# Optimization experiments

Measured on AMD Instinct MI355X. Metric: run time of the kernel, lower is better.

The kernel has to match this reference:

```python
import jax, jax.numpy as jnp
import numpy as np

N_NODES = 32768
N_EDGES = 524288
HID = 128


def _linear_params(key, fan_in, fan_out):
    kw, kb = jax.random.split(key)
    bound = 1.0 / np.sqrt(fan_in)
    w = jax.random.uniform(kw, (fan_in, fan_out), jnp.float32, -bound, bound)
    b = jax.random.uniform(kb, (fan_out,), jnp.float32, -bound, bound)
    return w, b


def setup_inputs() -> dict:
    key = jax.random.key(0)
    ks = jax.random.split(key, 8)
    x = jax.random.normal(ks[0], (N_NODES, HID), jnp.float32)
    edge_attr = jax.random.normal(ks[1], (N_EDGES, HID), jnp.float32)
    edges = jax.random.randint(ks[2], (2, N_EDGES), 0, N_NODES, jnp.int32)
    w1, b1 = _linear_params(ks[3], 3 * HID, HID)      # message_fn layer 1
    w2, b2 = _linear_params(ks[4], HID, HID)          # message_fn layer 2
    wu1, bu1 = _linear_params(ks[5], HID, 2 * HID)    # update_fn layer 1
    wu2, bu2 = _linear_params(ks[6], 2 * HID, HID)    # update_fn layer 2
    return {"x": x, "edge_attr": edge_attr, "edges": edges,
            "w1": w1, "b1": b1, "w2": w2, "b2": b2,
            "wu1": wu1, "bu1": bu1, "wu2": wu2, "bu2": bu2}


def reference(x, edge_attr, edges, w1, b1, w2, b2, wu1, bu1, wu2, bu2):
    n_nodes = x.shape[0]
    send, recv = edges[0], edges[1]
    # gather endpoint features and concat with edge attributes: [E, 3*HID]
    ea = jnp.concatenate([x[send], x[recv], edge_attr], axis=-1)
    # per-edge message MLP (Linear-SiLU-Linear-SiLU)
    h = jax.nn.silu(ea @ w1 + b1)
    msg = jax.nn.silu(h @ w2 + b2)                    # [E, HID]
    # scatter-mean into receiving nodes
    sums = jax.ops.segment_sum(msg, recv, num_segments=n_nodes)
    counts = jax.ops.segment_sum(jnp.ones((msg.shape[0],), msg.dtype), recv,
                                 num_segments=n_nodes)
    aggr = sums / jnp.maximum(counts, 1.0)[:, None]
    # residual (input_size == hidden_size -> Identity) + update MLP
    xo = x + aggr
    xo = xo + (jax.nn.silu(xo @ wu1 + bu1) @ wu2 + bu2)
    return xo, msg
```

## Files before the change

kernel.cpp:

```cpp
#include <hip/hip_runtime.h>
#include <hip/hip_bf16.h>

#define NN 32768
#define NE 524288
#define HID 128

typedef unsigned short u16;
typedef unsigned int u32;
typedef __bf16 bf16x8 __attribute__((ext_vector_type(8)));
typedef float f32x4 __attribute__((ext_vector_type(4)));

__device__ __forceinline__ u16 f2bf(float f) {
  union { float f; unsigned u; } v; v.f = f;
  return (u16)((v.u + 0x7fffu + ((v.u >> 16) & 1u)) >> 16);
}
__device__ __forceinline__ float silu_f(float v) {
  return v * __builtin_amdgcn_rcpf(1.f + __expf(-v));
}

__device__ __forceinline__ void gld16(const void* g, void* l) {
  __builtin_amdgcn_global_load_lds(
      (const __attribute__((address_space(1))) u32*)g,
      (__attribute__((address_space(3))) u32*)l, 16, 0, 0);
}

__global__ __launch_bounds__(256) void prep_k(
    const float* __restrict__ x, const float* __restrict__ w1,
    const float* __restrict__ w2, const float* __restrict__ wu1,
    const float* __restrict__ wu2,
    u16* __restrict__ xb, u16* __restrict__ w1Ts, u16* __restrict__ w2Ts,
    u16* __restrict__ wu1T, u16* __restrict__ wu2T, int* __restrict__ cnt)
{
  int i = blockIdx.x * 256 + threadIdx.x;
  xb[i] = f2bf(x[i]);
  if (i < NN) cnt[i] = 0;
  if (i < 3 * 128 * 128) {
    int j = i & 7, qs = (i >> 3) & 15, c = (i >> 7) & 127, s = i >> 14;
    int k = s * 128 + ((qs ^ (c & 7)) << 3) + j;
    w1Ts[i] = f2bf(w1[k * 128 + c]);
  }
  if (i < 128 * 128) {
    int j = i & 7, qs = (i >> 3) & 15, c = i >> 7;
    int k = ((qs ^ (c & 7)) << 3) + j;
    w2Ts[i] = f2bf(w2[k * 128 + c]);
  }
  if (i < 256 * 128) { int c = i >> 7, k = i & 127; wu1T[i] = f2bf(wu1[k * 256 + c]); }
  if (i < 128 * 256) { int c = i >> 8, k = i & 255; wu2T[i] = f2bf(wu2[k * 128 + c]); }
}

__global__ __launch_bounds__(256) void count_k(const int* __restrict__ recv,
                                               int* __restrict__ cnt)
{
  int e = blockIdx.x * 256 + threadIdx.x;
  atomicAdd(&cnt[recv[e]], 1);
}

__global__ __launch_bounds__(1024) void scan_k(const int* __restrict__ cnt,
                                               int* __restrict__ off,
                                               int* __restrict__ cursor)
{
  __shared__ int part[1024];
  const int tid = threadIdx.x;
  const int base = tid * 32;
  int v[32];
  int s = 0;
  #pragma unroll
  for (int j = 0; j < 32; ++j) { v[j] = cnt[base + j]; s += v[j]; }
  part[tid] = s;
  __syncthreads();
  #pragma unroll 1
  for (int d = 1; d < 1024; d <<= 1) {
    int t = (tid >= d) ? part[tid - d] : 0;
    __syncthreads();
    part[tid] += t;
    __syncthreads();
  }
  int ex = part[tid] - s;
  #pragma unroll
  for (int j = 0; j < 32; ++j) {
    off[base + j] = ex;
    cursor[base + j] = ex;
    ex += v[j];
  }
  if (tid == 1023) off[NN] = ex;
}

__global__ __launch_bounds__(256) void scatter_k(const int* __restrict__ recv,
                                                 int* __restrict__ cursor,
                                                 int* __restrict__ eperm)
{
  int e = blockIdx.x * 256 + threadIdx.x;
  int r = recv[e];
  int pos = atomicAdd(&cursor[r], 1);
  eperm[pos] = e;
}

__global__ __launch_bounds__(512, 4) void edge_mlp(
    const u16* __restrict__ xb, const float* __restrict__ eattr,
    const int* __restrict__ send, const int* __restrict__ recv,
    const u16* __restrict__ w1Ts, const float* __restrict__ b1,
    const u16* __restrict__ w2Ts, const float* __restrict__ b2,
    float* __restrict__ msg_out)
{
  __shared__ u16 sA[128 * 128];
  __shared__ u16 sB[128 * 128];

  const int tid  = threadIdx.x;
  const int lane = tid & 63;
  const int w    = tid >> 6;
  const int wr   = w >> 1;
  const int wc   = w & 1;
  const int fr   = lane & 15;
  const int fkq  = lane >> 4;
  const int orow = fkq * 4;
  const int e0   = blockIdx.x * 128;

  const int lrow4 = lane >> 4;
  const int schk  = lane & 15;

  int nds[4], ndr[4];
  #pragma unroll
  for (int i = 0; i < 4; ++i) {
    int e = e0 + w * 16 + i * 4 + lrow4;
    nds[i] = send[e];
    ndr[i] = recv[e];
  }

  f32x4 acc[2][4];
  #pragma unroll
  for (int m = 0; m < 2; ++m)
    #pragma unroll
    for (int n = 0; n < 4; ++n)
      #pragma unroll
      for (int r = 0; r < 4; ++r) acc[m][n][r] = 0.f;

  #pragma unroll
  for (int s = 0; s < 3; ++s) {
    if (s < 2) {
      #pragma unroll
      for (int i = 0; i < 4; ++i) {
        int rloc = w * 16 + i * 4 + lrow4;
        int node = (s == 0) ? nds[i] : ndr[i];
        gld16(xb + ((size_t)node << 7) + ((schk ^ (rloc & 7)) << 3),
              sA + ((w * 16 + i * 4) << 7));
      }
    } else {
      #pragma unroll
      for (int i = 0; i < 4; ++i) {
        int rloc = w * 16 + i * 4 + lrow4;
        int gchk = schk ^ (rloc & 7);
        const float4* p = reinterpret_cast<const float4*>(
            eattr + ((size_t)(e0 + rloc) << 7) + (gchk << 3));
        float4 v0 = p[0], v1 = p[1];
        uint4 d;
        d.x = (unsigned)f2bf(v0.x) | ((unsigned)f2bf(v0.y) << 16);
        d.y = (unsigned)f2bf(v0.z) | ((unsigned)f2bf(v0.w) << 16);
        d.z = (unsigned)f2bf(v1.x) | ((unsigned)f2bf(v1.y) << 16);
        d.w = (unsigned)f2bf(v1.z) | ((unsigned)f2bf(v1.w) << 16);
        *reinterpret_cast<uint4*>(sA + (rloc << 7) + (schk << 3)) = d;
      }
    }
    #pragma unroll
    for (int i = 0; i < 4; ++i) {
      gld16(w1Ts + ((size_t)s << 14) + ((w * 16 + i * 4) << 7) + (lane << 3),
            sB + ((w * 16 + i * 4) << 7));
    }
    __syncthreads();
    #pragma unroll
    for (int kk = 0; kk < 4; ++kk) {
      bf16x8 aF[2], bF[4];
      #pragma unroll
      for (int m = 0; m < 2; ++m) {
        int row = wr * 32 + m * 16 + fr;
        int ch = (kk * 4 + fkq) ^ (row & 7);
        aF[m] = __builtin_bit_cast(bf16x8,
            *reinterpret_cast<const uint4*>(sA + (row << 7) + (ch << 3)));
      }
      #pragma unroll
      for (int n = 0; n < 4; ++n) {
        int c = wc * 64 + n * 16 + fr;
        int ch = (kk * 4 + fkq) ^ (c & 7);
        bF[n] = __builtin_bit_cast(bf16x8,
            *reinterpret_cast<const uint4*>(sB + (c << 7) + (ch << 3)));
      }
      #pragma unroll
      for (int m = 0; m < 2; ++m)
        #pragma unroll
        for (int n = 0; n < 4; ++n)
          acc[m][n] = __builtin_amdgcn_mfma_f32_16x16x32_bf16(aF[m], bF[n], acc[m][n], 0, 0, 0);
    }
    __syncthreads();
  }

  #pragma unroll
  for (int n = 0; n < 4; ++n) {
    int c = wc * 64 + n * 16 + fr;
    float bb = b1[c];
    #pragma unroll
    for (int m = 0; m < 2; ++m) {
      #pragma unroll
      for (int r = 0; r < 4; ++r) {
        int row = wr * 32 + m * 16 + orow + r;
        sA[(row << 7) + (((c >> 3) ^ (row & 7)) << 3) + (c & 7)] =
            f2bf(silu_f(acc[m][n][r] + bb));
        acc[m][n][r] = 0.f;
      }
    }
  }
  #pragma unroll
  for (int i = 0; i < 4; ++i) {
    gld16(w2Ts + ((w * 16 + i * 4) << 7) + (lane << 3),
          sB + ((w * 16 + i * 4) << 7));
  }
  __syncthreads();

  #pragma unroll
  for (int kk = 0; kk < 4; ++kk) {
    bf16x8 aF[2], bF[4];
    #pragma unroll
    for (int m = 0; m < 2; ++m) {
      int row = wr * 32 + m * 16 + fr;
      int ch = (kk * 4 + fkq) ^ (row & 7);
      aF[m] = __builtin_bit_cast(bf16x8,
          *reinterpret_cast<const uint4*>(sA + (row << 7) + (ch << 3)));
    }
    #pragma unroll
    for (int n = 0; n < 4; ++n) {
      int c = wc * 64 + n * 16 + fr;
      int ch = (kk * 4 + fkq) ^ (c & 7);
      bF[n] = __builtin_bit_cast(bf16x8,
          *reinterpret_cast<const uint4*>(sB + (c << 7) + (ch << 3)));
    }
    #pragma unroll
    for (int m = 0; m < 2; ++m)
      #pragma unroll
      for (int n = 0; n < 4; ++n)
        acc[m][n] = __builtin_amdgcn_mfma_f32_16x16x32_bf16(aF[m], bF[n], acc[m][n], 0, 0, 0);
  }

  #pragma unroll
  for (int m = 0; m < 2; ++m) {
    #pragma unroll
    for (int r = 0; r < 4; ++r) {
      int e = e0 + wr * 32 + m * 16 + orow + r;
      #pragma unroll
      for (int n = 0; n < 4; ++n) {
        int c = wc * 64 + n * 16 + fr;
        msg_out[(size_t)e * HID + c] = silu_f(acc[m][n][r] + b2[c]);
      }
    }
  }
}

__global__ __launch_bounds__(256) void agg_k(
    const float* __restrict__ msg, const int* __restrict__ off,
    const int* __restrict__ eperm, const float* __restrict__ x,
    float* __restrict__ xin, u16* __restrict__ xob)
{
  const int wid = threadIdx.x >> 6, lane = threadIdx.x & 63;
  const int n = blockIdx.x * 4 + wid;
  const int j0 = off[n], j1 = off[n + 1];
  float ax = 0.f, ay = 0.f;
  int j = j0;
  for (; j + 1 < j1; j += 2) {
    int ea = eperm[j], eb = eperm[j + 1];
    float2 va = reinterpret_cast<const float2*>(msg + (size_t)ea * HID)[lane];
    float2 vb = reinterpret_cast<const float2*>(msg + (size_t)eb * HID)[lane];
    ax += va.x + vb.x;
    ay += va.y + vb.y;
  }
  if (j < j1) {
    int ea = eperm[j];
    float2 va = reinterpret_cast<const float2*>(msg + (size_t)ea * HID)[lane];
    ax += va.x; ay += va.y;
  }
  float inv = (j1 > j0) ? 1.f / (float)(j1 - j0) : 1.f;
  float2 xv = reinterpret_cast<const float2*>(x + (size_t)n * HID)[lane];
  float x0 = xv.x + ax * inv, x1 = xv.y + ay * inv;
  reinterpret_cast<float2*>(xin + (size_t)n * HID)[lane] = make_float2(x0, x1);
  reinterpret_cast<unsigned*>(xob)[n * 64 + lane] =
      (unsigned)f2bf(x0) | ((unsigned)f2bf(x1) << 16);
}

__global__ __launch_bounds__(256) void mlp1_k(
    const u16* __restrict__ xob, const u16* __restrict__ wu1T,
    const float* __restrict__ bu1, u16* __restrict__ t)
{
  __shared__ u16 sB[256][40];
  const int tid = threadIdx.x, lane = tid & 63, wid = tid >> 6;
  const int wr = wid >> 1, wc = wid & 1;
  const int fr = lane & 15, fk = (lane >> 4) * 8, orow = (lane >> 4) * 4;
  const int n0 = blockIdx.x * 64;

  f32x4 acc[2][8];
  #pragma unroll
  for (int m = 0; m < 2; ++m)
    #pragma unroll
    for (int n = 0; n < 8; ++n)
      #pragma unroll
      for (int r = 0; r < 4; ++r) acc[m][n][r] = 0.f;

  #pragma unroll 1
  for (int kk = 0; kk < 4; ++kk) {
    #pragma unroll
    for (int it = 0; it < 4; ++it) {
      int chunk = tid + it * 256;
      int c = chunk >> 2, q = chunk & 3;
      *reinterpret_cast<uint4*>(&sB[c][q * 8]) =
          *reinterpret_cast<const uint4*>(wu1T + c * 128 + kk * 32 + q * 8);
    }
    __syncthreads();
    bf16x8 aF[2], bF[8];
    #pragma unroll
    for (int m = 0; m < 2; ++m)
      aF[m] = __builtin_bit_cast(bf16x8, *reinterpret_cast<const uint4*>(
          xob + (size_t)(n0 + wr * 32 + m * 16 + fr) * HID + kk * 32 + fk));
    #pragma unroll
    for (int n = 0; n < 8; ++n)
      bF[n] = __builtin_bit_cast(bf16x8,
          *reinterpret_cast<const uint4*>(&sB[wc * 128 + n * 16 + fr][fk]));
    #pragma unroll
    for (int m = 0; m < 2; ++m)
      #pragma unroll
      for (int n = 0; n < 8; ++n)
        acc[m][n] = __builtin_amdgcn_mfma_f32_16x16x32_bf16(aF[m], bF[n], acc[m][n], 0, 0, 0);
    __syncthreads();
  }
  #pragma unroll
  for (int n = 0; n < 8; ++n) {
    int col = wc * 128 + n * 16 + fr;
    float bb = bu1[col];
    #pragma unroll
    for (int m = 0; m < 2; ++m) {
      int row = n0 + wr * 32 + m * 16 + orow;
      #pragma unroll
      for (int r = 0; r < 4; ++r)
        t[(size_t)(row + r) * 256 + col] = f2bf(silu_f(acc[m][n][r] + bb));
    }
  }
}

__global__ __launch_bounds__(256) void mlp2_k(
    const u16* __restrict__ t, const u16* __restrict__ wu2T,
    const float* __restrict__ bu2, const float* __restrict__ xin,
    float* __restrict__ xo)
{
  __shared__ u16 sB[128][40];
  const int tid = threadIdx.x, lane = tid & 63, wid = tid >> 6;
  const int wr = wid >> 1, wc = wid & 1;
  const int fr = lane & 15, fk = (lane >> 4) * 8, orow = (lane >> 4) * 4;
  const int n0 = blockIdx.x * 64;

  f32x4 acc[2][4];
  #pragma unroll
  for (int m = 0; m < 2; ++m)
    #pragma unroll
    for (int n = 0; n < 4; ++n)
      #pragma unroll
      for (int r = 0; r < 4; ++r) acc[m][n][r] = 0.f;

  #pragma unroll 1
  for (int kk = 0; kk < 8; ++kk) {
    #pragma unroll
    for (int it = 0; it < 2; ++it) {
      int chunk = tid + it * 256;
      int c = chunk >> 2, q = chunk & 3;
      *reinterpret_cast<uint4*>(&sB[c][q * 8]) =
          *reinterpret_cast<const uint4*>(wu2T + c * 256 + kk * 32 + q * 8);
    }
    __syncthreads();
    bf16x8 aF[2], bF[4];
    #pragma unroll
    for (int m = 0; m < 2; ++m)
      aF[m] = __builtin_bit_cast(bf16x8, *reinterpret_cast<const uint4*>(
          t + (size_t)(n0 + wr * 32 + m * 16 + fr) * 256 + kk * 32 + fk));
    #pragma unroll
    for (int n = 0; n < 4; ++n)
      bF[n] = __builtin_bit_cast(bf16x8,
          *reinterpret_cast<const uint4*>(&sB[wc * 64 + n * 16 + fr][fk]));
    #pragma unroll
    for (int m = 0; m < 2; ++m)
      #pragma unroll
      for (int n = 0; n < 4; ++n)
        acc[m][n] = __builtin_amdgcn_mfma_f32_16x16x32_bf16(aF[m], bF[n], acc[m][n], 0, 0, 0);
    __syncthreads();
  }
  #pragma unroll
  for (int m = 0; m < 2; ++m) {
    #pragma unroll
    for (int r = 0; r < 4; ++r) {
      int gn = n0 + wr * 32 + m * 16 + orow + r;
      #pragma unroll
      for (int n = 0; n < 4; ++n) {
        int col = wc * 64 + n * 16 + fr;
        xo[(size_t)gn * HID + col] =
            xin[(size_t)gn * HID + col] + acc[m][n][r] + bu2[col];
      }
    }
  }
}

extern "C" void kernel_launch(void* const* d_in, const int* in_sizes, int n_in,
                              void* d_out, int out_size, void* d_ws, size_t ws_size,
                              hipStream_t stream)
{
  (void)in_sizes; (void)n_in; (void)out_size; (void)ws_size;
  const float* x     = (const float*)d_in[0];
  const float* eattr = (const float*)d_in[1];
  const int*   edges = (const int*)d_in[2];
  const float* w1  = (const float*)d_in[3];
  const float* b1  = (const float*)d_in[4];
  const float* w2  = (const float*)d_in[5];
  const float* b2  = (const float*)d_in[6];
  const float* wu1 = (const float*)d_in[7];
  const float* bu1 = (const float*)d_in[8];
  const float* wu2 = (const float*)d_in[9];
  const float* bu2 = (const float*)d_in[10];

  float* xo  = (float*)d_out;
  float* msg = xo + (size_t)NN * HID;

  char* p = (char*)d_ws;
  u16* xb    = (u16*)p; p += (size_t)NN * HID * 2;
  u16* w1Ts  = (u16*)p; p += 384 * 128 * 2;
  u16* w2Ts  = (u16*)p; p += 128 * 128 * 2;
  u16* wu1T  = (u16*)p; p += 256 * 128 * 2;
  u16* wu2T  = (u16*)p; p += 128 * 256 * 2;
  u16* xob   = (u16*)p; p += (size_t)NN * HID * 2;
  u16* tbuf  = (u16*)p; p += (size_t)NN * 256 * 2;
  float* xin = (float*)p; p += (size_t)NN * HID * 4;
  int* cnt    = (int*)p; p += (size_t)NN * 4;
  int* off    = (int*)p; p += (size_t)(NN + 64) * 4;
  int* cursor = (int*)p; p += (size_t)NN * 4;
  int* eperm  = (int*)p; p += (size_t)NE * 4;

  const int* send = edges;
  const int* recv = edges + NE;

  prep_k<<<NN * HID / 256, 256, 0, stream>>>(x, w1, w2, wu1, wu2,
                                             xb, w1Ts, w2Ts, wu1T, wu2T, cnt);
  count_k<<<NE / 256, 256, 0, stream>>>(recv, cnt);
  scan_k<<<1, 1024, 0, stream>>>(cnt, off, cursor);
  scatter_k<<<NE / 256, 256, 0, stream>>>(recv, cursor, eperm);
  edge_mlp<<<NE / 128, 512, 0, stream>>>(xb, eattr, send, recv,
                                         w1Ts, b1, w2Ts, b2, msg);
  agg_k<<<NN / 4, 256, 0, stream>>>(msg, off, eperm, x, xin, xob);
  mlp1_k<<<NN / 64, 256, 0, stream>>>(xob, wu1T, bu1, tbuf);
  mlp2_k<<<NN / 64, 256, 0, stream>>>(tbuf, wu2T, bu2, xin, xo);
}
```

Before: 339.4 us.

## Restructure edge MLP to read weights from global and gather both endpoints up front

The edge MLP now gathers sender and receiver features into two LDS buffers in one phase. Weight fragments are read directly from global/L2 instead of being staged through LDS. Edge attributes are converted in registers and fed straight to MFMA, the warp tiling changes to 2x4, and priority hints are set around the MFMA blocks. The count kernel is folded into prep with a memset, the aggregation loop is unrolled to 4, and the node MLPs drop LDS weight staging and its barriers. These changes aim to cut barriers, LDS traffic and launches, at the cost of more global weight loads per wave and more register pressure.

Measured after the change: 546.3 us. 1.61x slower.

```diff
diff --git a/kernel.cpp b/kernel.cpp
--- a/kernel.cpp
+++ b/kernel.cpp
@@ -11,11 +11,16 @@
 typedef float f32x4 __attribute__((ext_vector_type(4)));
 
 __device__ __forceinline__ u16 f2bf(float f) {
-  union { float f; unsigned u; } v; v.f = f;
-  return (u16)((v.u + 0x7fffu + ((v.u >> 16) & 1u)) >> 16);
+  return __builtin_bit_cast(u16, (__bf16)f);
 }
 __device__ __forceinline__ float silu_f(float v) {
   return v * __builtin_amdgcn_rcpf(1.f + __expf(-v));
+}
+__device__ __forceinline__ bf16x8 cvt8(float4 a, float4 b) {
+  bf16x8 r;
+  r[0] = (__bf16)a.x; r[1] = (__bf16)a.y; r[2] = (__bf16)a.z; r[3] = (__bf16)a.w;
+  r[4] = (__bf16)b.x; r[5] = (__bf16)b.y; r[6] = (__bf16)b.z; r[7] = (__bf16)b.w;
+  return r;
 }
 
 __device__ __forceinline__ void gld16(const void* g, void* l) {
@@ -27,32 +32,20 @@
 __global__ __launch_bounds__(256) void prep_k(
     const float* __restrict__ x, const float* __restrict__ w1,
     const float* __restrict__ w2, const float* __restrict__ wu1,
-    const float* __restrict__ wu2,
-    u16* __restrict__ xb, u16* __restrict__ w1Ts, u16* __restrict__ w2Ts,
+    const float* __restrict__ wu2, const int* __restrict__ recv,
+    u16* __restrict__ xb, u16* __restrict__ w1T, u16* __restrict__ w2T,
     u16* __restrict__ wu1T, u16* __restrict__ wu2T, int* __restrict__ cnt)
 {
   int i = blockIdx.x * 256 + threadIdx.x;
   xb[i] = f2bf(x[i]);
-  if (i < NN) cnt[i] = 0;
+  if (i < NE) atomicAdd(&cnt[recv[i]], 1);
   if (i < 3 * 128 * 128) {
-    int j = i & 7, qs = (i >> 3) & 15, c = (i >> 7) & 127, s = i >> 14;
-    int k = s * 128 + ((qs ^ (c & 7)) << 3) + j;
-    w1Ts[i] = f2bf(w1[k * 128 + c]);
-  }
-  if (i < 128 * 128) {
-    int j = i & 7, qs = (i >> 3) & 15, c = i >> 7;
-    int k = ((qs ^ (c & 7)) << 3) + j;
-    w2Ts[i] = f2bf(w2[k * 128 + c]);
-  }
-  if (i < 256 * 128) { int c = i >> 7, k = i & 127; wu1T[i] = f2bf(wu1[k * 256 + c]); }
-  if (i < 128 * 256) { int c = i >> 8, k = i & 255; wu2T[i] = f2bf(wu2[k * 128 + c]); }
-}
-
-__global__ __launch_bounds__(256) void count_k(const int* __restrict__ recv,
-                                               int* __restrict__ cnt)
-{
-  int e = blockIdx.x * 256 + threadIdx.x;
-  atomicAdd(&cnt[recv[e]], 1);
+    int k = i & 127, c = (i >> 7) & 127, s = i >> 14;
+    w1T[i] = f2bf(w1[(s * 128 + k) * 128 + c]);
+  }
+  if (i < 128 * 128) { int k = i & 127, c = i >> 7; w2T[i]  = f2bf(w2[k * 128 + c]); }
+  if (i < 256 * 128) { int k = i & 127, c = i >> 7; wu1T[i] = f2bf(wu1[k * 256 + c]); }
+  if (i < 128 * 256) { int k = i & 255, c = i >> 8; wu2T[i] = f2bf(wu2[k * 128 + c]); }
 }
 
 __global__ __launch_bounds__(1024) void scan_k(const int* __restrict__ cnt,
@@ -98,18 +91,17 @@
 __global__ __launch_bounds__(512, 4) void edge_mlp(
     const u16* __restrict__ xb, const float* __restrict__ eattr,
     const int* __restrict__ send, const int* __restrict__ recv,
-    const u16* __restrict__ w1Ts, const float* __restrict__ b1,
-    const u16* __restrict__ w2Ts, const float* __restrict__ b2,
+    const u16* __restrict__ w1T, const float* __restrict__ b1,
+    const u16* __restrict__ w2T, const float* __restrict__ b2,
     float* __restrict__ msg_out)
 {
-  __shared__ u16 sA[128 * 128];
-  __shared__ u16 sB[128 * 128];
+  __shared__ u16 sA[2][128 * 128];
 
   const int tid  = threadIdx.x;
   const int lane = tid & 63;
   const int w    = tid >> 6;
-  const int wr   = w >> 1;
-  const int wc   = w & 1;
+  const int wr   = w >> 2;
+  const int wc   = w & 3;
   const int fr   = lane & 15;
   const int fkq  = lane >> 4;
   const int orow = fkq * 4;
@@ -118,137 +110,136 @@
   const int lrow4 = lane >> 4;
   const int schk  = lane & 15;
 
-  int nds[4], ndr[4];
+  float b1v[2] = { b1[wc * 32 + fr], b1[wc * 32 + 16 + fr] };
+  float b2v[2] = { b2[wc * 32 + fr], b2[wc * 32 + 16 + fr] };
+
   #pragma unroll
   for (int i = 0; i < 4; ++i) {
-    int e = e0 + w * 16 + i * 4 + lrow4;
-    nds[i] = send[e];
-    ndr[i] = recv[e];
-  }
-
-  f32x4 acc[2][4];
-  #pragma unroll
-  for (int m = 0; m < 2; ++m)
-    #pragma unroll
-    for (int n = 0; n < 4; ++n)
+    int rloc = w * 16 + i * 4 + lrow4;
+    int gchk = (schk ^ (rloc & 7)) << 3;
+    int ns = send[e0 + rloc], nr = recv[e0 + rloc];
+    gld16(xb + ((size_t)ns << 7) + gchk, &sA[0][(w * 16 + i * 4) << 7]);
+    gld16(xb + ((size_t)nr << 7) + gchk, &sA[1][(w * 16 + i * 4) << 7]);
+  }
+
+  f32x4 acc[4][2];
+  #pragma unroll
+  for (int m = 0; m < 4; ++m)
+    #pragma unroll
+    for (int n = 0; n < 2; ++n)
       #pragma unroll
       for (int r = 0; r < 4; ++r) acc[m][n][r] = 0.f;
 
-  #pragma unroll
-  for (int s = 0; s < 3; ++s) {
-    if (s < 2) {
-      #pragma unroll
-      for (int i = 0; i < 4; ++i) {
-        int rloc = w * 16 + i * 4 + lrow4;
-        int node = (s == 0) ? nds[i] : ndr[i];
-        gld16(xb + ((size_t)node << 7) + ((schk ^ (rloc & 7)) << 3),
-              sA + ((w * 16 + i * 4) << 7));
-      }
-    } else {
-      #pragma unroll
-      for (int i = 0; i < 4; ++i) {
-        int rloc = w * 16 + i * 4 + lrow4;
-        int gchk = schk ^ (rloc & 7);
-        const float4* p = reinterpret_cast<const float4*>(
-            eattr + ((size_t)(e0 + rloc) << 7) + (gchk << 3));
-        float4 v0 = p[0], v1 = p[1];
-        uint4 d;
-        d.x = (unsigned)f2bf(v0.x) | ((unsigned)f2bf(v0.y) << 16);
-        d.y = (unsigned)f2bf(v0.z) | ((unsigned)f2bf(v0.w) << 16);
-        d.z = (unsigned)f2bf(v1.x) | ((unsigned)f2bf(v1.y) << 16);
-        d.w = (unsigned)f2bf(v1.z) | ((unsigned)f2bf(v1.w) << 16);
-        *reinterpret_cast<uint4*>(sA + (rloc << 7) + (schk << 3)) = d;
-      }
-    }
-    #pragma unroll
-    for (int i = 0; i < 4; ++i) {
-      gld16(w1Ts + ((size_t)s << 14) + ((w * 16 + i * 4) << 7) + (lane << 3),
-            sB + ((w * 16 + i * 4) << 7));
-    }
-    __syncthreads();
+  __syncthreads();
+
+  #pragma unroll
+  for (int s = 0; s < 2; ++s) {
+    const u16* buf = sA[s];
+    const u16* wp  = w1T + ((size_t)s << 14) + ((wc * 32 + fr) << 7) + fkq * 8;
     #pragma unroll
     for (int kk = 0; kk < 4; ++kk) {
-      bf16x8 aF[2], bF[4];
-      #pragma unroll
-      for (int m = 0; m < 2; ++m) {
-        int row = wr * 32 + m * 16 + fr;
+      bf16x8 bF[2], aF[4];
+      #pragma unroll
+      for (int n = 0; n < 2; ++n)
+        bF[n] = __builtin_bit_cast(bf16x8,
+            *reinterpret_cast<const uint4*>(wp + n * 2048 + kk * 32));
+      #pragma unroll
+      for (int m = 0; m < 4; ++m) {
+        int row = wr * 64 + m * 16 + fr;
         int ch = (kk * 4 + fkq) ^ (row & 7);
         aF[m] = __builtin_bit_cast(bf16x8,
-            *reinterpret_cast<const uint4*>(sA + (row << 7) + (ch << 3)));
-      }
-      #pragma unroll
-      for (int n = 0; n < 4; ++n) {
-        int c = wc * 64 + n * 16 + fr;
-        int ch = (kk * 4 + fkq) ^ (c & 7);
+            *reinterpret_cast<const uint4*>(buf + (row << 7) + (ch << 3)));
+      }
+      __builtin_amdgcn_s_setprio(1);
+      #pragma unroll
+      for (int m = 0; m < 4; ++m)
+        #pragma unroll
+        for (int n = 0; n < 2; ++n)
+          acc[m][n] = __builtin_amdgcn_mfma_f32_16x16x32_bf16(aF[m], bF[n], acc[m][n], 0, 0, 0);
+      __builtin_amdgcn_s_setprio(0);
+    }
+  }
+
+  {
+    const u16* wp = w1T + (2 << 14) + ((wc * 32 + fr) << 7) + fkq * 8;
+    #pragma unroll
+    for (int m = 0; m < 4; ++m) {
+      const float* ep = eattr + ((size_t)(e0 + wr * 64 + m * 16 + fr) << 7) + fkq * 8;
+      float4 r0[4], r1[4];
+      #pragma unroll
+      for (int kk = 0; kk < 4; ++kk) {
+        r0[kk] = *reinterpret_cast<const float4*>(ep + kk * 32);
+        r1[kk] = *reinterpret_cast<const float4*>(ep + kk * 32 + 4);
+      }
+      #pragma unroll
+      for (int kk = 0; kk < 4; ++kk) {
+        bf16x8 aF = cvt8(r0[kk], r1[kk]);
+        bf16x8 bF[2];
+        #pragma unroll
+        for (int n = 0; n < 2; ++n)
+          bF[n] = __builtin_bit_cast(bf16x8,
+              *reinterpret_cast<const uint4*>(wp + n * 2048 + kk * 32));
+        __builtin_amdgcn_s_setprio(1);
+        #pragma unroll
+        for (int n = 0; n < 2; ++n)
+          acc[m][n] = __builtin_amdgcn_mfma_f32_16x16x32_bf16(aF, bF[n], acc[m][n], 0, 0, 0);
+        __builtin_amdgcn_s_setprio(0);
+      }
+    }
+  }
+
+  __syncthreads();
+
+  #pragma unroll
+  for (int m = 0; m < 4; ++m) {
+    #pragma unroll
+    for (int n = 0; n < 2; ++n) {
+      int c = wc * 32 + n * 16 + fr;
+      #pragma unroll
+      for (int r = 0; r < 4; ++r) {
+        int row = wr * 64 + m * 16 + orow + r;
+        sA[0][(row << 7) + (((c >> 3) ^ (row & 7)) << 3) + (c & 7)] =
+            f2bf(silu_f(acc[m][n][r] + b1v[n]));
+        acc[m][n][r] = 0.f;
+      }
+    }
+  }
+  __syncthreads();
+
+  {
+    const u16* wp = w2T + ((wc * 32 + fr) << 7) + fkq * 8;
+    #pragma unroll
+    for (int kk = 0; kk < 4; ++kk) {
+      bf16x8 bF[2], aF[4];
+      #pragma unroll
+      for (int n = 0; n < 2; ++n)
         bF[n] = __builtin_bit_cast(bf16x8,
-            *reinterpret_cast<const uint4*>(sB + (c << 7) + (ch << 3)));
-      }
-      #pragma unroll
-      for (int m = 0; m < 2; ++m)
+            *reinterpret_cast<const uint4*>(wp + n * 2048 + kk * 32));
+      #pragma unroll
+      for (int m = 0; m < 4; ++m) {
+        int row = wr * 64 + m * 16 + fr;
+        int ch = (kk * 4 + fkq) ^ (row & 7);
+        aF[m] = __builtin_bit_cast(bf16x8,
+            *reinterpret_cast<const uint4*>(sA[0] + (row << 7) + (ch << 3)));
+      }
+      __builtin_amdgcn_s_setprio(1);
+      #pragma unroll
+      for (int m = 0; m < 4; ++m)
         #pragma unroll
-        for (int n = 0; n < 4; ++n)
+        for (int n = 0; n < 2; ++n)
           acc[m][n] = __builtin_amdgcn_mfma_f32_16x16x32_bf16(aF[m], bF[n], acc[m][n], 0, 0, 0);
-    }
-    __syncthreads();
-  }
-
-  #pragma unroll
-  for (int n = 0; n < 4; ++n) {
-    int c = wc * 64 + n * 16 + fr;
-    float bb = b1[c];
-    #pragma unroll
-    for (int m = 0; m < 2; ++m) {
-      #pragma unroll
-      for (int r = 0; r < 4; ++r) {
-        int row = wr * 32 + m * 16 + orow + r;
-        sA[(row << 7) + (((c >> 3) ^ (row & 7)) << 3) + (c & 7)] =
-            f2bf(silu_f(acc[m][n][r] + bb));
-        acc[m][n][r] = 0.f;
-      }
-    }
-  }
-  #pragma unroll
-  for (int i = 0; i < 4; ++i) {
-    gld16(w2Ts + ((w * 16 + i * 4) << 7) + (lane << 3),
-          sB + ((w * 16 + i * 4) << 7));
-  }
-  __syncthreads();
-
-  #pragma unroll
-  for (int kk = 0; kk < 4; ++kk) {
-    bf16x8 aF[2], bF[4];
-    #pragma unroll
-    for (int m = 0; m < 2; ++m) {
-      int row = wr * 32 + m * 16 + fr;
-      int ch = (kk * 4 + fkq) ^ (row & 7);
-      aF[m] = __builtin_bit_cast(bf16x8,
-          *reinterpret_cast<const uint4*>(sA + (row << 7) + (ch << 3)));
-    }
-    #pragma unroll
-    for (int n = 0; n < 4; ++n) {
-      int c = wc * 64 + n * 16 + fr;
-      int ch = (kk * 4 + fkq) ^ (c & 7);
-      bF[n] = __builtin_bit_cast(bf16x8,
-          *reinterpret_cast<const uint4*>(sB + (c << 7) + (ch << 3)));
-    }
-    #pragma unroll
-    for (int m = 0; m < 2; ++m)
-      #pragma unroll
-      for (int n = 0; n < 4; ++n)
-        acc[m][n] = __builtin_amdgcn_mfma_f32_16x16x32_bf16(aF[m], bF[n], acc[m][n], 0, 0, 0);
-  }
-
-  #pragma unroll
-  for (int m = 0; m < 2; ++m) {
-    #pragma unroll
-    for (int r = 0; r < 4; ++r) {
-      int e = e0 + wr * 32 + m * 16 + orow + r;
-      #pragma unroll
-      for (int n = 0; n < 4; ++n) {
-        int c = wc * 64 + n * 16 + fr;
-        msg_out[(size_t)e * HID + c] = silu_f(acc[m][n][r] + b2[c]);
-      }
-    }
+      __builtin_amdgcn_s_setprio(0);
+    }
+  }
+
+  #pragma unroll
+  for (int m = 0; m < 4; ++m) {
+    float* mp = msg_out + ((size_t)(e0 + wr * 64 + m * 16 + orow) << 7) + wc * 32 + fr;
+    #pragma unroll
+    for (int r = 0; r < 4; ++r)
+      #pragma unroll
+      for (int n = 0; n < 2; ++n)
+        mp[r * 128 + n * 16] = silu_f(acc[m][n][r] + b2v[n]);
   }
 }
 
@@ -262,14 +253,16 @@
   const int j0 = off[n], j1 = off[n + 1];
   float ax = 0.f, ay = 0.f;
   int j = j0;
-  for (; j + 1 < j1; j += 2) {
-    int ea = eperm[j], eb = eperm[j + 1];
+  for (; j + 3 < j1; j += 4) {
+    int ea = eperm[j], eb = eperm[j + 1], ec = eperm[j + 2], ed = eperm[j + 3];
     float2 va = reinterpret_cast<const float2*>(msg + (size_t)ea * HID)[lane];
     float2 vb = reinterpret_cast<const float2*>(msg + (size_t)eb * HID)[lane];
-    ax += va.x + vb.x;
-    ay += va.y + vb.y;
-  }
-  if (j < j1) {
+    float2 vc = reinterpret_cast<const float2*>(msg + (size_t)ec * HID)[lane];
+    float2 vd = reinterpret_cast<const float2*>(msg + (size_t)ed * HID)[lane];
+    ax += (va.x + vb.x) + (vc.x + vd.x);
+    ay += (va.y + vb.y) + (vc.y + vd.y);
+  }
+  for (; j < j1; ++j) {
     int ea = eperm[j];
     float2 va = reinterpret_cast<const float2*>(msg + (size_t)ea * HID)[lane];
     ax += va.x; ay += va.y;
@@ -282,14 +275,13 @@
       (unsigned)f2bf(x0) | ((unsigned)f2bf(x1) << 16);
 }
 
-__global__ __launch_bounds__(256) void mlp1_k(
+__global__ __launch_bounds__(256, 4) void mlp1_k(
     const u16* __restrict__ xob, const u16* __restrict__ wu1T,
     const float* __restrict__ bu1, u16* __restrict__ t)
 {
-  __shared__ u16 sB[256][40];
   const int tid = threadIdx.x, lane = tid & 63, wid = tid >> 6;
   const int wr = wid >> 1, wc = wid & 1;
-  const int fr = lane & 15, fk = (lane >> 4) * 8, orow = (lane >> 4) * 4;
+  const int fr = lane & 15, fkq = lane >> 4, orow = fkq * 4;
   const int n0 = blockIdx.x * 64;
 
   f32x4 acc[2][8];
@@ -300,31 +292,25 @@
       #pragma unroll
       for (int r = 0; r < 4; ++r) acc[m][n][r] = 0.f;
 
-  #pragma unroll 1
+  const u16* wp = wu1T + ((wc * 128 + fr) << 7) + fkq * 8;
+  #pragma unroll
   for (int kk = 0; kk < 4; ++kk) {
-    #pragma unroll
-    for (int it = 0; it < 4; ++it) {
-      int chunk = tid + it * 256;
-      int c = chunk >> 2, q = chunk & 3;
-      *reinterpret_cast<uint4*>(&sB[c][q * 8]) =
-          *reinterpret_cast<const uint4*>(wu1T + c * 128 + kk * 32 + q * 8);
-    }
-    __syncthreads();
     bf16x8 aF[2], bF[8];
     #pragma unroll
     for (int m = 0; m < 2; ++m)
       aF[m] = __builtin_bit_cast(bf16x8, *reinterpret_cast<const uint4*>(
-          xob + (size_t)(n0 + wr * 32 + m * 16 + fr) * HID + kk * 32 + fk));
+          xob + ((size_t)(n0 + wr * 32 + m * 16 + fr) << 7) + kk * 32 + fkq * 8));
     #pragma unroll
     for (int n = 0; n < 8; ++n)
       bF[n] = __builtin_bit_cast(bf16x8,
-          *reinterpret_cast<const uint4*>(&sB[wc * 128 + n * 16 + fr][fk]));
+          *reinterpret_cast<const uint4*>(wp + n * 2048 + kk * 32));
+    __builtin_amdgcn_s_setprio(1);
     #pragma unroll
     for (int m = 0; m < 2; ++m)
       #pragma unroll
       for (int n = 0; n < 8; ++n)
         acc[m][n] = __builtin_amdgcn_mfma_f32_16x16x32_bf16(aF[m], bF[n], acc[m][n], 0, 0, 0);
-    __syncthreads();
+    __builtin_amdgcn_s_setprio(0);
   }
   #pragma unroll
   for (int n = 0; n < 8; ++n) {
@@ -340,15 +326,14 @@
   }
 }
 
-__global__ __launch_bounds__(256) void mlp2_k(
+__global__ __launch_bounds__(256, 4) void mlp2_k(
     const u16* __restrict__ t, const u16* __restrict__ wu2T,
     const float* __restrict__ bu2, const float* __restrict__ xin,
     float* __restrict__ xo)
 {
-  __shared__ u16 sB[128][40];
   const int tid = threadIdx.x, lane = tid & 63, wid = tid >> 6;
   const int wr = wid >> 1, wc = wid & 1;
-  const int fr = lane & 15, fk = (lane >> 4) * 8, orow = (lane >> 4) * 4;
+  const int fr = lane & 15, fkq = lane >> 4, orow = fkq * 4;
   const int n0 = blockIdx.x * 64;
 
   f32x4 acc[2][4];
@@ -359,31 +344,25 @@
       #pragma unroll
       for (int r = 0; r < 4; ++r) acc[m][n][r] = 0.f;
 
-  #pragma unroll 1
+  const u16* wp = wu2T + (size_t)(wc * 64 + fr) * 256 + fkq * 8;
+  #pragma unroll
   for (int kk = 0; kk < 8; ++kk) {
-    #pragma unroll
-    for (int it = 0; it < 2; ++it) {
-      int chunk = tid + it * 256;
-      int c = chunk >> 2, q = chunk & 3;
-      *reinterpret_cast<uint4*>(&sB[c][q * 8]) =
-          *reinterpret_cast<const uint4*>(wu2T + c * 256 + kk * 32 + q * 8);
-    }
-    __syncthreads();
     bf16x8 aF[2], bF[4];
     #pragma unroll
     for (int m = 0; m < 2; ++m)
       aF[m] = __builtin_bit_cast(bf16x8, *reinterpret_cast<const uint4*>(
-          t + (size_t)(n0 + wr * 32 + m * 16 + fr) * 256 + kk * 32 + fk));
+          t + (size_t)(n0 + wr * 32 + m * 16 + fr) * 256 + kk * 32 + fkq * 8));
     #pragma unroll
     for (int n = 0; n < 4; ++n)
       bF[n] = __builtin_bit_cast(bf16x8,
-          *reinterpret_cast<const uint4*>(&sB[wc * 64 + n * 16 + fr][fk]));
+          *reinterpret_cast<const uint4*>(wp + n * 4096 + kk * 32));
+    __builtin_amdgcn_s_setprio(1);
     #pragma unroll
     for (int m = 0; m < 2; ++m)
       #pragma unroll
       for (int n = 0; n < 4; ++n)
         acc[m][n] = __builtin_amdgcn_mfma_f32_16x16x32_bf16(aF[m], bF[n], acc[m][n], 0, 0, 0);
-    __syncthreads();
+    __builtin_amdgcn_s_setprio(0);
   }
   #pragma unroll
   for (int m = 0; m < 2; ++m) {
@@ -422,8 +401,8 @@
 
   char* p = (char*)d_ws;
   u16* xb    = (u16*)p; p += (size_t)NN * HID * 2;
-  u16* w1Ts  = (u16*)p; p += 384 * 128 * 2;
-  u16* w2Ts  = (u16*)p; p += 128 * 128 * 2;
+  u16* w1T   = (u16*)p; p += 384 * 128 * 2;
+  u16* w2T   = (u16*)p; p += 128 * 128 * 2;
   u16* wu1T  = (u16*)p; p += 256 * 128 * 2;
   u16* wu2T  = (u16*)p; p += 128 * 256 * 2;
   u16* xob   = (u16*)p; p += (size_t)NN * HID * 2;
@@ -437,13 +416,13 @@
   const int* send = edges;
   const int* recv = edges + NE;
 
-  prep_k<<<NN * HID / 256, 256, 0, stream>>>(x, w1, w2, wu1, wu2,
-                                             xb, w1Ts, w2Ts, wu1T, wu2T, cnt);
-  count_k<<<NE / 256, 256, 0, stream>>>(recv, cnt);
+  hipMemsetAsync(cnt, 0, (size_t)NN * 4, stream);
+  prep_k<<<NN * HID / 256, 256, 0, stream>>>(x, w1, w2, wu1, wu2, recv,
+                                             xb, w1T, w2T, wu1T, wu2T, cnt);
   scan_k<<<1, 1024, 0, stream>>>(cnt, off, cursor);
   scatter_k<<<NE / 256, 256, 0, stream>>>(recv, cursor, eperm);
   edge_mlp<<<NE / 128, 512, 0, stream>>>(xb, eattr, send, recv,
-                                         w1Ts, b1, w2Ts, b2, msg);
+                                         w1T, b1, w2T, b2, msg);
   agg_k<<<NN / 4, 256, 0, stream>>>(msg, off, eperm, x, xin, xob);
   mlp1_k<<<NN / 64, 256, 0, stream>>>(xob, wu1T, bu1, tbuf);
   mlp2_k<<<NN / 64, 256, 0, stream>>>(tbuf, wu2T, bu2, xin, xo);
```
